# Optimization experiments

Hardware: AMD Instinct MI355X
Metric: run time of the kernel (lower is better)

Reference implementation:

```python
import jax, jax.numpy as jnp
import numpy as np

CLIP_TANH = 10.0
M_CHECKS, N_VARS = 256, 512   # parity-check matrix shape
ROW_W = 8                     # ones per check row -> E = 256*8 = 2048 edges
BATCH = 16384


def _build_masks():
    """Tanner-graph connectivity masks, as in init_w_skipconn2even / initialize_w_v2c."""
    rng = np.random.default_rng(0)
    pcm = np.zeros((M_CHECKS, N_VARS), np.float32)
    for r in range(M_CHECKS):
        pcm[r, rng.choice(N_VARS, ROW_W, replace=False)] = 1.0
    checks, variables = np.nonzero(pcm)  # edge list, row-major order, length E
    E = checks.size
    # edge e' feeds edge e iff same variable node, different check node
    same_var = variables[:, None] == variables[None, :]
    diff_chk = checks[:, None] != checks[None, :]
    w_odd2even_mask = (same_var & diff_chk).astype(np.float32)               # [E, E]
    # variable v feeds every edge incident to it
    w_skip_mask = (np.arange(N_VARS)[:, None] == variables[None, :]).astype(np.float32)  # [N, E]
    return jnp.asarray(w_odd2even_mask), jnp.asarray(w_skip_mask), E


def setup_inputs() -> dict:
    key = jax.random.key(0)
    w_o2e_mask, w_skip_mask, E = _build_masks()
    k = jax.random.split(key, 5)
    return {
        "x": jax.random.normal(k[0], (BATCH, E), jnp.float32),          # edge messages
        "llr": jax.random.normal(k[1], (BATCH, N_VARS), jnp.float32),   # channel LLRs
        "u": jax.random.uniform(k[2], (E,), jnp.float32),               # dropout uniforms
        "odd_weights": 0.05 * jax.random.normal(k[3], (E, E), jnp.float32),
        "llr_weights": 1.0 + 0.05 * jax.random.normal(k[4], (N_VARS, E), jnp.float32),
        "dropout_logits": 10.0 * jnp.ones((E,), jnp.float32),           # 10000*LOGITS_INIT analogue (sigmoid ~ 1)
        "w_odd2even_mask": w_o2e_mask,
        "w_skipconn2even_mask": w_skip_mask,
    }


def reference(x, llr, u, odd_weights, llr_weights, dropout_logits,
              w_odd2even_mask, w_skipconn2even_mask):
    # TEST-phase forward, mask_only=False
    total_mask = w_odd2even_mask * odd_weights                        # [E, E], very sparse support
    z = (u < jax.nn.sigmoid(dropout_logits)).astype(x.dtype)          # Bernoulli gate per source edge
    mask_after_dropout = total_mask * z[:, None]                      # row-wise gating
    msg = x @ mask_after_dropout                                      # [B, E]
    skip = llr @ (w_skipconn2even_mask * llr_weights)                 # [B, E]
    odd_clamp = jnp.clip(msg + skip, -CLIP_TANH, CLIP_TANH)
    return jnp.tanh(0.5 * odd_clamp)
```

## Files before the change

### kernel.cpp

```cpp
#include <hip/hip_runtime.h>
#include <hip/hip_bf16.h>

constexpr int E     = 2048;
constexpr int NVARS = 512;
constexpr int DMAX  = 20;
constexpr int TB    = 8;
constexpr int NT    = 512;

__device__ __forceinline__ unsigned bf16hi(float f) {
    const unsigned uu = __float_as_uint(f);
    return (uu + 0x7FFFu + ((uu >> 16) & 1u)) & 0xFFFF0000u;
}
__device__ __forceinline__ unsigned cvtpk(float lo, float hi) {
    unsigned r;
    asm("v_cvt_pk_bf16_f32 %0, %1, %2" : "=v"(r) : "v"(lo), "v"(hi));
    return r;
}
__device__ __forceinline__ float bl(unsigned q) { return __uint_as_float(q << 16); }
__device__ __forceinline__ float bh(unsigned q) { return __uint_as_float(q & 0xFFFF0000u); }

__global__ __launch_bounds__(256)
void k_vsrc(const float* __restrict__ skip_mask,
            const float* __restrict__ llr_w,
            unsigned short* __restrict__ vsrc,
            float* __restrict__ skw)
{
    const int col = blockIdx.x * 256 + threadIdx.x;
    const int v0  = blockIdx.y * (NVARS / 32);
    for (int v = v0; v < v0 + NVARS / 32; ++v) {
        const float m = skip_mask[(size_t)v * E + col];
        if (m != 0.0f) {
            vsrc[col] = (unsigned short)v;
            skw [col] = m * llr_w[(size_t)v * E + col];
        }
    }
}

__global__ __launch_bounds__(64)
void k_pervar(const unsigned short* __restrict__ vsrc,
              const float* __restrict__ skw,
              const float* __restrict__ odd_w,
              const float* __restrict__ u,
              const float* __restrict__ logits,
              uint4*  __restrict__ wtc,
              float4* __restrict__ hdr,
              int*    __restrict__ nitems)
{
    __shared__ unsigned short vs[E];
    __shared__ int deg[NVARS];
    __shared__ unsigned short mem[DMAX];
    __shared__ float zf[DMAX];
    __shared__ float sks[DMAX];

    const int v   = blockIdx.x;
    const int tid = threadIdx.x;

    for (int i = tid; i < E / 8; i += 64)
        ((uint4*)vs)[i] = ((const uint4*)vsrc)[i];
    for (int i = tid; i < NVARS; i += 64) deg[i] = 0;
    __syncthreads();
    for (int i = tid; i < E; i += 64) atomicAdd(&deg[vs[i]], 1);
    __syncthreads();

    const int dv = deg[v];

    int itot = 0, ib = 0, wb = 0;
    for (int i = tid; i < NVARS; i += 64) {
        const int d2 = deg[i];
        if (!d2) continue;
        const int dc = (d2 < DMAX) ? d2 : DMAX;
        const int ic = (dc + 3) >> 2;
        itot += ic;
        if (dv > 0 && (d2 < dv || (d2 == dv && i < v))) { ib += ic; wb += dc * ic; }
    }
    #pragma unroll
    for (int o = 32; o; o >>= 1) {
        itot += __shfl_xor(itot, o);
        ib   += __shfl_xor(ib,   o);
        wb   += __shfl_xor(wb,   o);
    }
    if (v == 0 && tid == 0) nitems[0] = itot;
    if (!dv) return;
    const int de = (dv < DMAX) ? dv : DMAX;
    const int ic = (de + 3) >> 2;

    int cnt = 0;
    for (int c = 0; c < E / 64; ++c) {
        const int e = c * 64 + tid;
        const bool m = ((int)vs[e] == v);
        const unsigned long long bal = __ballot(m);
        if (m) {
            const int pos = cnt + __popcll(bal & ((1ull << tid) - 1ull));
            if (pos < DMAX) mem[pos] = (unsigned short)e;
        }
        cnt += __popcll(bal);
    }
    __syncthreads();

    if (tid < de) {
        const int m = mem[tid];
        const float sig = 1.0f / (1.0f + __expf(-logits[m]));
        zf [tid] = (u[m] < sig) ? 1.0f : 0.0f;
        sks[tid] = skw[m];
    }
    __syncthreads();

    if (tid < ic) {
        const int o0 = tid * 4;
        float s0 = 0, s1 = 0, s2 = 0, s3 = 0;
        unsigned c0 = 0xFFFFu, c1 = 0xFFFFu, c2 = 0xFFFFu, c3 = 0xFFFFu;
        if (o0 + 0 < de) { s0 = sks[o0 + 0]; c0 = mem[o0 + 0]; }
        if (o0 + 1 < de) { s1 = sks[o0 + 1]; c1 = mem[o0 + 1]; }
        if (o0 + 2 < de) { s2 = sks[o0 + 2]; c2 = mem[o0 + 2]; }
        if (o0 + 3 < de) { s3 = sks[o0 + 3]; c3 = mem[o0 + 3]; }
        hdr[2 * (ib + tid)]     = make_float4(s0, s1, s2, s3);
        hdr[2 * (ib + tid) + 1] = make_float4(
            __uint_as_float(c0 | (c1 << 16)),
            __uint_as_float(c2 | (c3 << 16)),
            __uint_as_float((unsigned)(wb + tid * de)),
            __uint_as_float((unsigned)v | ((unsigned)de << 16)));
    }

    for (int idx = tid; idx < de * ic; idx += 64) {
        const int k = idx / de;
        const int j = idx - k * de;
        const int src = mem[j];
        unsigned g[4];
        #pragma unroll
        for (int q = 0; q < 4; ++q) {
            const int o = 4 * k + q;
            float ww = 0.0f;
            if (o < de && o != j)
                ww = odd_w[(size_t)src * E + mem[o]] * zf[j];
            g[q] = bf16hi(ww) | (unsigned)src;
        }
        wtc[wb + idx] = make_uint4(g[0], g[1], g[2], g[3]);
    }
}

__device__ __forceinline__ float th(float s) {
    float c = fminf(fmaxf(s, -10.0f), 10.0f);
    float t = __expf(c);
    return (t - 1.0f) * __builtin_amdgcn_rcpf(t + 1.0f);
}

__global__ __launch_bounds__(NT, 6)
void fused_main(const float* __restrict__ x,
                const float* __restrict__ llr,
                const uint4*  __restrict__ wtc,
                const float4* __restrict__ hdr,
                const int*    __restrict__ nitems,
                float* __restrict__ out)
{
    __shared__ uint4 xs[E];
    __shared__ uint4 ls[NVARS];

    const int b0 = blockIdx.x * TB;
    const int t  = threadIdx.x;

    {
        const float4* xr = (const float4*)(x + (size_t)b0 * E);
        const float4 r0 = xr[0 * (E / 4) + t];
        const float4 r1 = xr[1 * (E / 4) + t];
        const float4 r2 = xr[2 * (E / 4) + t];
        const float4 r3 = xr[3 * (E / 4) + t];
        const float4 r4 = xr[4 * (E / 4) + t];
        const float4 r5 = xr[5 * (E / 4) + t];
        const float4 r6 = xr[6 * (E / 4) + t];
        const float4 r7 = xr[7 * (E / 4) + t];
        xs[4 * t + 0] = make_uint4(cvtpk(r0.x, r1.x), cvtpk(r2.x, r3.x),
                                   cvtpk(r4.x, r5.x), cvtpk(r6.x, r7.x));
        xs[4 * t + 1] = make_uint4(cvtpk(r0.y, r1.y), cvtpk(r2.y, r3.y),
                                   cvtpk(r4.y, r5.y), cvtpk(r6.y, r7.y));
        xs[4 * t + 2] = make_uint4(cvtpk(r0.z, r1.z), cvtpk(r2.z, r3.z),
                                   cvtpk(r4.z, r5.z), cvtpk(r6.z, r7.z));
        xs[4 * t + 3] = make_uint4(cvtpk(r0.w, r1.w), cvtpk(r2.w, r3.w),
                                   cvtpk(r4.w, r5.w), cvtpk(r6.w, r7.w));
    }
    {
        const float* lr = llr + (size_t)b0 * NVARS;
        ls[t] = make_uint4(cvtpk(lr[t],             lr[NVARS + t]),
                           cvtpk(lr[2 * NVARS + t], lr[3 * NVARS + t]),
                           cvtpk(lr[4 * NVARS + t], lr[5 * NVARS + t]),
                           cvtpk(lr[6 * NVARS + t], lr[7 * NVARS + t]));
    }
    __syncthreads();

    const int nit = nitems[0];

    unsigned sst[2][4][4];
    unsigned scc[2][2];

    #pragma unroll
    for (int r = 0; r < 2; ++r) {
        scc[r][0] = 0xFFFFFFFFu;
        scc[r][1] = 0xFFFFFFFFu;
        const int it = r * NT + t;
        if (it < nit) {
            const float4 ha = hdr[2 * it];
            const uint4  hb = ((const uint4*)hdr)[2 * it + 1];
            const unsigned woff = hb.z;
            const int v = hb.w & 0xFFFF;
            const int d = hb.w >> 16;

            const uint4 lvq = ls[v];
            const float lf0 = bl(lvq.x), lf1 = bh(lvq.x);
            const float lf2 = bl(lvq.y), lf3 = bh(lvq.y);
            const float lf4 = bl(lvq.z), lf5 = bh(lvq.z);
            const float lf6 = bl(lvq.w), lf7 = bh(lvq.w);

            float a[4][8];
            #pragma unroll
            for (int ii = 0; ii < 4; ++ii) {
                const float sk = (ii == 0) ? ha.x : (ii == 1) ? ha.y
                               : (ii == 2) ? ha.z : ha.w;
                a[ii][0] = sk * lf0; a[ii][1] = sk * lf1;
                a[ii][2] = sk * lf2; a[ii][3] = sk * lf3;
                a[ii][4] = sk * lf4; a[ii][5] = sk * lf5;
                a[ii][6] = sk * lf6; a[ii][7] = sk * lf7;
            }

            const uint4* wp = wtc + woff;
            for (int j = 0; j < d; ++j) {
                const uint4 g = wp[j];
                const int   s = (int)(g.x & 0x7FFu);
                const uint4 xv = xs[s];
                const float w0 = bh(g.x), w1 = bh(g.y);
                const float w2 = bh(g.z), w3 = bh(g.w);
                const float xf0 = bl(xv.x), xf1 = bh(xv.x);
                const float xf2 = bl(xv.y), xf3 = bh(xv.y);
                const float xf4 = bl(xv.z), xf5 = bh(xv.z);
                const float xf6 = bl(xv.w), xf7 = bh(xv.w);
                a[0][0] += w0 * xf0; a[0][1] += w0 * xf1;
                a[0][2] += w0 * xf2; a[0][3] += w0 * xf3;
                a[0][4] += w0 * xf4; a[0][5] += w0 * xf5;
                a[0][6] += w0 * xf6; a[0][7] += w0 * xf7;
                a[1][0] += w1 * xf0; a[1][1] += w1 * xf1;
                a[1][2] += w1 * xf2; a[1][3] += w1 * xf3;
                a[1][4] += w1 * xf4; a[1][5] += w1 * xf5;
                a[1][6] += w1 * xf6; a[1][7] += w1 * xf7;
                a[2][0] += w2 * xf0; a[2][1] += w2 * xf1;
                a[2][2] += w2 * xf2; a[2][3] += w2 * xf3;
                a[2][4] += w2 * xf4; a[2][5] += w2 * xf5;
                a[2][6] += w2 * xf6; a[2][7] += w2 * xf7;
                a[3][0] += w3 * xf0; a[3][1] += w3 * xf1;
                a[3][2] += w3 * xf2; a[3][3] += w3 * xf3;
                a[3][4] += w3 * xf4; a[3][5] += w3 * xf5;
                a[3][6] += w3 * xf6; a[3][7] += w3 * xf7;
            }

            scc[r][0] = hb.x;
            scc[r][1] = hb.y;
            #pragma unroll
            for (int ii = 0; ii < 4; ++ii) {
                sst[r][ii][0] = cvtpk(th(a[ii][0]), th(a[ii][1]));
                sst[r][ii][1] = cvtpk(th(a[ii][2]), th(a[ii][3]));
                sst[r][ii][2] = cvtpk(th(a[ii][4]), th(a[ii][5]));
                sst[r][ii][3] = cvtpk(th(a[ii][6]), th(a[ii][7]));
            }
        }
    }

    __syncthreads();
    unsigned* osp = (unsigned*)xs;
    #pragma unroll
    for (int r = 0; r < 2; ++r) {
        #pragma unroll
        for (int ii = 0; ii < 4; ++ii) {
            const unsigned c = (scc[r][ii >> 1] >> ((ii & 1) * 16)) & 0xFFFFu;
            if (c != 0xFFFFu) {
                osp[0 * E + c] = sst[r][ii][0];
                osp[1 * E + c] = sst[r][ii][1];
                osp[2 * E + c] = sst[r][ii][2];
                osp[3 * E + c] = sst[r][ii][3];
            }
        }
    }
    __syncthreads();

    #pragma unroll
    for (int k = 0; k < E / NT; ++k) {
        const int e = k * NT + t;
        #pragma unroll
        for (int p = 0; p < 4; ++p) {
            const unsigned q = osp[p * E + e];
            out[(size_t)(b0 + 2 * p) * E + e]     = bl(q);
            out[(size_t)(b0 + 2 * p + 1) * E + e] = bh(q);
        }
    }
}

extern "C" void kernel_launch(void* const* d_in, const int* in_sizes, int n_in,
                              void* d_out, int out_size, void* d_ws, size_t ws_size,
                              hipStream_t stream) {
    const float* x        = (const float*)d_in[0];
    const float* llr      = (const float*)d_in[1];
    const float* u        = (const float*)d_in[2];
    const float* odd_w    = (const float*)d_in[3];
    const float* llr_w    = (const float*)d_in[4];
    const float* logits   = (const float*)d_in[5];
    const float* skip_msk = (const float*)d_in[7];
    float* out = (float*)d_out;

    const int B = in_sizes[0] / E;

    char* wsb = (char*)d_ws;
    size_t off = 0;
    uint4*          wtc  = (uint4*)(wsb + off);          off += (size_t)6144 * 16;
    float4*         hdr  = (float4*)(wsb + off);         off += (size_t)1024 * 32;
    float*          skw  = (float*)(wsb + off);          off += (size_t)E * 4;
    unsigned short* vsrc = (unsigned short*)(wsb + off); off += (size_t)E * 2;
    int*            nit  = (int*)(wsb + off);            off += 16;

    k_vsrc  <<<dim3(E / 256, 32), dim3(256), 0, stream>>>(skip_msk, llr_w, vsrc, skw);
    k_pervar<<<dim3(NVARS),       dim3(64),  0, stream>>>(vsrc, skw, odd_w, u, logits,
                                                          wtc, hdr, nit);

    fused_main<<<dim3(B / TB), dim3(NT), 0, stream>>>(x, llr, wtc, hdr, nit, out);
}
```

Measured before the change: 91.74 us.

## Halve batch tile, load inputs via global_load_lds in fp32, vectorize output stores

Cuts the per-block batch tile from 8 to 4 rows and stages x and llr into LDS as fp32 with direct global-to-LDS DMA loads, replacing the register-staged bf16 transpose-and-pack. The inner loop now does four scalar LDS reads per source edge instead of one packed uint4 read. Output is written with float4 stores, and the occupancy hint rises to 8 blocks. The aim is lower register pressure, more occupancy and less conversion work, at the cost of more blocks, twice as many weight-table reads overall, and more LDS read instructions per edge.

```diff
diff --git a/kernel.cpp b/kernel.cpp
--- a/kernel.cpp
+++ b/kernel.cpp
@@ -4,7 +4,7 @@
 constexpr int E     = 2048;
 constexpr int NVARS = 512;
 constexpr int DMAX  = 20;
-constexpr int TB    = 8;
+constexpr int TB    = 4;
 constexpr int NT    = 512;
 
 __device__ __forceinline__ unsigned bf16hi(float f) {
@@ -18,6 +18,9 @@
 }
 __device__ __forceinline__ float bl(unsigned q) { return __uint_as_float(q << 16); }
 __device__ __forceinline__ float bh(unsigned q) { return __uint_as_float(q & 0xFFFF0000u); }
+
+typedef const __attribute__((address_space(1))) void* gas_t;
+typedef __attribute__((address_space(3))) void*       las_t;
 
 __global__ __launch_bounds__(256)
 void k_vsrc(const float* __restrict__ skip_mask,
@@ -144,7 +147,7 @@
     return (t - 1.0f) * __builtin_amdgcn_rcpf(t + 1.0f);
 }
 
-__global__ __launch_bounds__(NT, 6)
+__global__ __launch_bounds__(NT, 8)
 void fused_main(const float* __restrict__ x,
                 const float* __restrict__ llr,
                 const uint4*  __restrict__ wtc,
@@ -152,43 +155,34 @@
                 const int*    __restrict__ nitems,
                 float* __restrict__ out)
 {
-    __shared__ uint4 xs[E];
-    __shared__ uint4 ls[NVARS];
-
-    const int b0 = blockIdx.x * TB;
-    const int t  = threadIdx.x;
+    __shared__ float xsf[TB * E];
+    __shared__ float lsf[TB * NVARS];
+
+    const int b0   = blockIdx.x * TB;
+    const int t    = threadIdx.x;
+    const int wid  = t >> 6;
+    const int lane = t & 63;
 
     {
-        const float4* xr = (const float4*)(x + (size_t)b0 * E);
-        const float4 r0 = xr[0 * (E / 4) + t];
-        const float4 r1 = xr[1 * (E / 4) + t];
-        const float4 r2 = xr[2 * (E / 4) + t];
-        const float4 r3 = xr[3 * (E / 4) + t];
-        const float4 r4 = xr[4 * (E / 4) + t];
-        const float4 r5 = xr[5 * (E / 4) + t];
-        const float4 r6 = xr[6 * (E / 4) + t];
-        const float4 r7 = xr[7 * (E / 4) + t];
-        xs[4 * t + 0] = make_uint4(cvtpk(r0.x, r1.x), cvtpk(r2.x, r3.x),
-                                   cvtpk(r4.x, r5.x), cvtpk(r6.x, r7.x));
-        xs[4 * t + 1] = make_uint4(cvtpk(r0.y, r1.y), cvtpk(r2.y, r3.y),
-                                   cvtpk(r4.y, r5.y), cvtpk(r6.y, r7.y));
-        xs[4 * t + 2] = make_uint4(cvtpk(r0.z, r1.z), cvtpk(r2.z, r3.z),
-                                   cvtpk(r4.z, r5.z), cvtpk(r6.z, r7.z));
-        xs[4 * t + 3] = make_uint4(cvtpk(r0.w, r1.w), cvtpk(r2.w, r3.w),
-                                   cvtpk(r4.w, r5.w), cvtpk(r6.w, r7.w));
-    }
-    {
-        const float* lr = llr + (size_t)b0 * NVARS;
-        ls[t] = make_uint4(cvtpk(lr[t],             lr[NVARS + t]),
-                           cvtpk(lr[2 * NVARS + t], lr[3 * NVARS + t]),
-                           cvtpk(lr[4 * NVARS + t], lr[5 * NVARS + t]),
-                           cvtpk(lr[6 * NVARS + t], lr[7 * NVARS + t]));
+        const float* gx = x + (size_t)b0 * E;
+        #pragma unroll
+        for (int rr = 0; rr < 4; ++rr) {
+            const int cbase = wid * 256 + rr * 64;
+            const float* gp = gx + (size_t)(cbase + lane) * 4;
+            __builtin_amdgcn_global_load_lds(
+                (gas_t)gp, (las_t)((char*)xsf + (size_t)cbase * 16), 16, 0, 0);
+        }
+        const float* gl = llr + (size_t)b0 * NVARS;
+        const int cbase = wid * 64;
+        const float* gp = gl + (size_t)(cbase + lane) * 4;
+        __builtin_amdgcn_global_load_lds(
+            (gas_t)gp, (las_t)((char*)lsf + (size_t)cbase * 16), 16, 0, 0);
     }
     __syncthreads();
 
     const int nit = nitems[0];
 
-    unsigned sst[2][4][4];
+    unsigned sst[2][4][2];
     unsigned scc[2][2];
 
     #pragma unroll
@@ -199,54 +193,41 @@
         if (it < nit) {
             const float4 ha = hdr[2 * it];
             const uint4  hb = ((const uint4*)hdr)[2 * it + 1];
-            const unsigned woff = hb.z;
+            const uint4* wp = wtc + hb.z;
             const int v = hb.w & 0xFFFF;
             const int d = hb.w >> 16;
 
-            const uint4 lvq = ls[v];
-            const float lf0 = bl(lvq.x), lf1 = bh(lvq.x);
-            const float lf2 = bl(lvq.y), lf3 = bh(lvq.y);
-            const float lf4 = bl(lvq.z), lf5 = bh(lvq.z);
-            const float lf6 = bl(lvq.w), lf7 = bh(lvq.w);
-
-            float a[4][8];
+            const float lf0 = lsf[0 * NVARS + v];
+            const float lf1 = lsf[1 * NVARS + v];
+            const float lf2 = lsf[2 * NVARS + v];
+            const float lf3 = lsf[3 * NVARS + v];
+
+            float a[4][4];
             #pragma unroll
             for (int ii = 0; ii < 4; ++ii) {
                 const float sk = (ii == 0) ? ha.x : (ii == 1) ? ha.y
                                : (ii == 2) ? ha.z : ha.w;
                 a[ii][0] = sk * lf0; a[ii][1] = sk * lf1;
                 a[ii][2] = sk * lf2; a[ii][3] = sk * lf3;
-                a[ii][4] = sk * lf4; a[ii][5] = sk * lf5;
-                a[ii][6] = sk * lf6; a[ii][7] = sk * lf7;
-            }
-
-            const uint4* wp = wtc + woff;
+            }
+
             for (int j = 0; j < d; ++j) {
                 const uint4 g = wp[j];
                 const int   s = (int)(g.x & 0x7FFu);
-                const uint4 xv = xs[s];
+                const float xf0 = xsf[0 * E + s];
+                const float xf1 = xsf[1 * E + s];
+                const float xf2 = xsf[2 * E + s];
+                const float xf3 = xsf[3 * E + s];
                 const float w0 = bh(g.x), w1 = bh(g.y);
                 const float w2 = bh(g.z), w3 = bh(g.w);
-                const float xf0 = bl(xv.x), xf1 = bh(xv.x);
-                const float xf2 = bl(xv.y), xf3 = bh(xv.y);
-                const float xf4 = bl(xv.z), xf5 = bh(xv.z);
-                const float xf6 = bl(xv.w), xf7 = bh(xv.w);
                 a[0][0] += w0 * xf0; a[0][1] += w0 * xf1;
                 a[0][2] += w0 * xf2; a[0][3] += w0 * xf3;
-                a[0][4] += w0 * xf4; a[0][5] += w0 * xf5;
-                a[0][6] += w0 * xf6; a[0][7] += w0 * xf7;
                 a[1][0] += w1 * xf0; a[1][1] += w1 * xf1;
                 a[1][2] += w1 * xf2; a[1][3] += w1 * xf3;
-                a[1][4] += w1 * xf4; a[1][5] += w1 * xf5;
-                a[1][6] += w1 * xf6; a[1][7] += w1 * xf7;
                 a[2][0] += w2 * xf0; a[2][1] += w2 * xf1;
                 a[2][2] += w2 * xf2; a[2][3] += w2 * xf3;
-                a[2][4] += w2 * xf4; a[2][5] += w2 * xf5;
-                a[2][6] += w2 * xf6; a[2][7] += w2 * xf7;
                 a[3][0] += w3 * xf0; a[3][1] += w3 * xf1;
                 a[3][2] += w3 * xf2; a[3][3] += w3 * xf3;
-                a[3][4] += w3 * xf4; a[3][5] += w3 * xf5;
-                a[3][6] += w3 * xf6; a[3][7] += w3 * xf7;
             }
 
             scc[r][0] = hb.x;
@@ -255,14 +236,12 @@
             for (int ii = 0; ii < 4; ++ii) {
                 sst[r][ii][0] = cvtpk(th(a[ii][0]), th(a[ii][1]));
                 sst[r][ii][1] = cvtpk(th(a[ii][2]), th(a[ii][3]));
-                sst[r][ii][2] = cvtpk(th(a[ii][4]), th(a[ii][5]));
-                sst[r][ii][3] = cvtpk(th(a[ii][6]), th(a[ii][7]));
-            }
-        }
-    }
-
-    __syncthreads();
-    unsigned* osp = (unsigned*)xs;
+            }
+        }
+    }
+
+    __syncthreads();
+    unsigned* osp = (unsigned*)xsf;
     #pragma unroll
     for (int r = 0; r < 2; ++r) {
         #pragma unroll
@@ -271,22 +250,19 @@
             if (c != 0xFFFFu) {
                 osp[0 * E + c] = sst[r][ii][0];
                 osp[1 * E + c] = sst[r][ii][1];
-                osp[2 * E + c] = sst[r][ii][2];
-                osp[3 * E + c] = sst[r][ii][3];
-            }
-        }
-    }
-    __syncthreads();
-
-    #pragma unroll
-    for (int k = 0; k < E / NT; ++k) {
-        const int e = k * NT + t;
-        #pragma unroll
-        for (int p = 0; p < 4; ++p) {
-            const unsigned q = osp[p * E + e];
-            out[(size_t)(b0 + 2 * p) * E + e]     = bl(q);
-            out[(size_t)(b0 + 2 * p + 1) * E + e] = bh(q);
-        }
+            }
+        }
+    }
+    __syncthreads();
+
+    #pragma unroll
+    for (int i = 0; i < 4; ++i) {
+        const int p = i >> 1, hf = i & 1;
+        const uint4 w4 = ((const uint4*)(osp + p * E))[t];
+        float4 o;
+        if (hf == 0) o = make_float4(bl(w4.x), bl(w4.y), bl(w4.z), bl(w4.w));
+        else         o = make_float4(bh(w4.x), bh(w4.y), bh(w4.z), bh(w4.w));
+        ((float4*)(out + (size_t)(b0 + i) * E))[t] = o;
     }
 }
 
```

Measured after the change: 103.6 us. +12.9%, slower.
